# Performance work log

Hardware: AMD Instinct MI355X
Metric: run time of the kernel (lower is better)

Reference implementation:

```python
import jax, jax.numpy as jnp
import numpy as np

N_QUBITS = 12
N_LAYERS = 2
PATCH = 16
NPS = 14  # patches per side for 224/16
N_PATCHES = NPS * NPS
SCALE = 1.0 / np.sqrt(N_QUBITS)


def _butterfly_gates(n):
    # Faithful replication of QuantumOrthogonalLayer.butterfly_circuit indexing:
    # param_idx increments even when the (idx1, idx2) pair is skipped.
    gates, pidx = [], 0
    n_bl = int(np.ceil(np.log2(n)))
    for layer in range(n_bl):
        stride = 2 ** layer
        for start in range(0, n - stride, 2 * stride):
            for off in range(stride):
                i1, i2 = start + off, start + off + stride
                if i1 < n and i2 < n:
                    gates.append((pidx, i1, i2))
                pidx += 1
    nppl = sum(2 ** (n_bl - 1 - i) * 2 ** i for i in range(n_bl))  # n_params() = 32
    return gates, nppl

GATES, NPPL = _butterfly_gates(N_QUBITS)

# Pauli-Z sign table: qubit 0 is the most-significant bit of the flattened state index.
_bits = (np.arange(2 ** N_QUBITS)[:, None] >> np.arange(N_QUBITS - 1, -1, -1)[None, :]) & 1
Z_SIGNS = jnp.asarray(1.0 - 2.0 * _bits, dtype=jnp.float32)  # (4096, 12)


def _rbs_u(theta):
    # 4x4 real unitary of RY(2t,w1); CNOT(w1,w2); RY(-2t,w1); CNOT(w1,w2)
    c, s = jnp.cos(theta), jnp.sin(theta)
    c2, s2, cs = c * c, s * s, c * s
    return jnp.stack([
        jnp.stack([c2, s2, -cs, cs]),
        jnp.stack([s2, c2, cs, -cs]),
        jnp.stack([cs, -cs, c2, s2]),
        jnp.stack([-cs, cs, s2, c2]),
    ])


def _apply_2q(state, U, i, j):
    # state: (P, 2, 2, ..., 2); apply U to qubit axes i, j
    st = jnp.moveaxis(state, (1 + i, 1 + j), (-2, -1))
    shp = st.shape
    st = st.reshape(shp[:-2] + (4,)) @ U.T
    return jnp.moveaxis(st.reshape(shp), (-2, -1), (1 + i, 1 + j))


@jax.checkpoint
def quantum_expvals(features, params):
    # features: (P, n_qubits) angles; params: (N_LAYERS * NPPL,)
    P = features.shape[0]
    half = 0.5 * features
    amp = jnp.stack([jnp.cos(half), jnp.sin(half)], axis=-1)  # (P, n, 2) RY(x)|0>
    state = jnp.ones((P, 1), features.dtype)
    for q in range(N_QUBITS):  # product-state angle encoding
        state = (state[:, :, None] * amp[:, q][:, None, :]).reshape(P, -1)
    state = state.reshape((P,) + (2,) * N_QUBITS)
    for l in range(N_LAYERS):
        base = l * NPPL
        for pidx, w1, w2 in GATES:
            state = _apply_2q(state, _rbs_u(params[base + pidx]), w1, w2)
    probs = state.reshape(P, -1) ** 2
    return probs @ Z_SIGNS  # (P, n_qubits) <Z_i>


def setup_inputs() -> dict:
    key = jax.random.key(0)
    ks = jax.random.split(key, 6)
    x = jax.random.normal(ks[0], (4, 3, 224, 224), dtype=jnp.float32)
    W_proj = jax.random.normal(ks[1], (N_QUBITS, PATCH * PATCH), dtype=jnp.float32) / np.sqrt(PATCH * PATCH)
    b_proj = jnp.zeros((N_QUBITS,), jnp.float32)
    q_params = 0.1 * jax.random.normal(ks[2], (N_LAYERS * NPPL,), dtype=jnp.float32)
    k_params = 0.1 * jax.random.normal(ks[3], (N_LAYERS * NPPL,), dtype=jnp.float32)
    v_params = 0.1 * jax.random.normal(ks[4], (N_LAYERS * NPPL,), dtype=jnp.float32)
    W_cls = jax.random.normal(ks[5], (1000, N_PATCHES * N_QUBITS), dtype=jnp.float32) / np.sqrt(N_PATCHES * N_QUBITS)
    b_cls = jnp.zeros((1000,), jnp.float32)
    return {"x": x, "W_proj": W_proj, "b_proj": b_proj, "q_params": q_params,
            "k_params": k_params, "v_params": v_params, "W_cls": W_cls, "b_cls": b_cls}


def reference(x, W_proj, b_proj, q_params, k_params, v_params, W_cls, b_cls):
    B = x.shape[0]
    xg = jnp.mean(x, axis=1)  # channel average -> (B, H, W)
    patches = xg.reshape(B, NPS, PATCH, NPS, PATCH).transpose(0, 1, 3, 2, 4)
    patches = patches.reshape(B, N_PATCHES, PATCH * PATCH)
    proj = patches @ W_proj.T + b_proj  # (B, n_patches, n_qubits)
    feats = proj.reshape(-1, N_QUBITS)
    Q = quantum_expvals(feats, q_params).reshape(B, N_PATCHES, N_QUBITS)
    K = quantum_expvals(feats, k_params).reshape(B, N_PATCHES, N_QUBITS)
    V = quantum_expvals(feats, v_params).reshape(B, N_PATCHES, N_QUBITS)
    attn = jax.nn.softmax(jnp.einsum('bqd,bkd->bqk', Q, K) * SCALE, axis=-1)
    out = jnp.einsum('bqk,bkd->bqd', attn, V)  # (B, n_patches, n_qubits)
    logits = out.reshape(B, -1) @ W_cls.T + b_cls
    return logits
```

## Files before the change

kernel.cpp:

```cpp
#include <hip/hip_runtime.h>
#include <math.h>

#define NQ        12
#define NPS       14
#define NPATCH    196
#define NB        4
#define NCLS      1000
#define FEATDIM   2352
#define SCALE_F   0.28867513459481287f

typedef float v2f __attribute__((ext_vector_type(2)));

constexpr int PRa[8][5] = {
    {2,3,0,1, 4},
    {2,3,4,5, 6},
    {2,3,5,6, 7},
    {2,3,0,4, 6},
    {2,3,8,9,10},
    {2,3,9,10,11},
    {2,3,0,8,10},
    {2,3,1,5, 9},
};
constexpr int PTa[8][7] = {
    {5,6,7,8,9,10,11},
    {7,0,1,8,9,10,11},
    {0,1,4,8,9,10,11},
    {8,9,10,1,5,7,11},
    {4,0,1,5,6,7,11},
    {0,1,8,5,6,7,4},
    {1,5,9,6,7,11,4},
    {6,0,11,7,8,10,4},
};
constexpr bool BARa[8] = {false,false,false,false,true,false,false,true};

constexpr int cwgt(int X, int q) {
    for (int k = 0; k < 5; ++k) if (PRa[X][k] == q) return 1 << k;
    for (int m = 0; m < 7; ++m) if (PTa[X][m] == q) return 36 << m;
    return 0;
}
constexpr int rimmB(int X, int Y, int a) {
    int s = 0;
    for (int j = 0; j < 3; ++j)
        if ((a >> j) & 1) s += cwgt(X, PRa[Y][2 + j]);
    return s;
}

template<int TI>
__device__ __forceinline__ void relayoutB(v2f amp2[16], float* lds, int tid, int base) {
    constexpr int X = TI, Y = (TI + 1) & 7;
    float4* dst = (float4*)(lds + 36 * tid);
    #pragma unroll
    for (int k = 0; k < 8; ++k)
        dst[k] = make_float4(amp2[2*k][0], amp2[2*k][1], amp2[2*k+1][0], amp2[2*k+1][1]);
    if (BARa[TI]) __syncthreads();
    #pragma unroll
    for (int a = 0; a < 8; ++a) {
        float4 v = *(const float4*)(lds + base + rimmB(X, Y, a));
        amp2[2*a][0] = v.x; amp2[2*a][1] = v.y;
        amp2[2*a+1][0] = v.z; amp2[2*a+1][1] = v.w;
    }
    if (BARa[TI]) __syncthreads();
}

template<int MI, int MJ>
__device__ __forceinline__ void pk_gate(v2f a[16], float gc, float gs) {
    v2f H = {0.5f, 0.5f}, C = {gc, gc}, S = {gs, gs};
    #pragma unroll
    for (int m = 0; m < 16; ++m) {
        if (m & (MI | MJ)) continue;
        v2f a0 = a[m], a1 = a[m | MJ], a2 = a[m | MI], a3 = a[m | MI | MJ];
        v2f p  = a0 + a1, q  = a0 - a1;
        v2f p2 = a2 + a3, q2 = a2 - a3;
        v2f t1 = H * p  + C * q  - S * q2;
        v2f t2 = H * p2 + C * q2 + S * q;
        a[m]           = t1;
        a[m | MJ]      = p  - t1;
        a[m | MI]      = t2;
        a[m | MI | MJ] = p2 - t2;
    }
}

template<int MI, int MJ>
__device__ __forceinline__ void sc_gate(float* amp, float gc, float gs) {
    #pragma unroll
    for (int m = 0; m < 32; ++m) {
        if (m & (MI | MJ)) continue;
        float a0 = amp[m], a1 = amp[m | MJ], a2 = amp[m | MI], a3 = amp[m | MI | MJ];
        float p  = a0 + a1, q  = a0 - a1;
        float p2 = a2 + a3, q2 = a2 - a3;
        float t1 = 0.5f * p  + gc * q  - gs * q2;
        float t2 = 0.5f * p2 + gc * q2 + gs * q;
        amp[m]           = t1;
        amp[m | MJ]      = p  - t1;
        amp[m | MI]      = t2;
        amp[m | MI | MJ] = p2 - t2;
    }
}

template<int CTRL>
__device__ __forceinline__ float dppadd(float x) {
    int s = __builtin_amdgcn_update_dpp(0, __float_as_int(x), CTRL, 0xf, 0xf, true);
    return x + __int_as_float(s);
}
__device__ __forceinline__ float wave_sum(float x) {
    x = dppadd<0x111>(x);
    x = dppadd<0x112>(x);
    x = dppadd<0x114>(x);
    x = dppadd<0x118>(x);
    x = dppadd<0x142>(x);
    x = dppadd<0x143>(x);
    return x;
}

__global__ __launch_bounds__(128, 4) void qcirc_kernel(
    const float* __restrict__ x,
    const float* __restrict__ Wp,
    const float* __restrict__ bproj,
    const float* __restrict__ qp,
    const float* __restrict__ kp,
    const float* __restrict__ vp,
    float* __restrict__ qkv)
{
    __shared__ __align__(16) float lds[4608];
    __shared__ float chs[NQ], shs[NQ];
    __shared__ float gC[40], gS[40];
    __shared__ float red2[2][12];

    const int tid = threadIdx.x;
    const int p = blockIdx.x, b = blockIdx.y, c = blockIdx.z;
    const int bp = b * NPATCH + p;
    const float* params = (c == 0) ? qp : (c == 1) ? kp : vp;
    const int lane = tid & 63, wv = tid >> 6;

    float part[NQ];
    #pragma unroll
    for (int q = 0; q < NQ; ++q) part[q] = 0.0f;
    {
        int py = p / NPS, px = p % NPS;
        const float* xb = x + (size_t)b * 3 * 224 * 224;
        #pragma unroll
        for (int k = 0; k < 2; ++k) {
            int pix = tid + 128 * k;
            int off = (py * 16 + (pix >> 4)) * 224 + px * 16 + (pix & 15);
            float v = (xb[off] + xb[off + 50176] + xb[off + 100352]) * (1.0f / 3.0f);
            #pragma unroll
            for (int q = 0; q < NQ; ++q) part[q] += v * Wp[q * 256 + pix];
        }
    }
    if (tid < 40) {
        int l = tid / 20, g = tid - l * 20;
        float th = params[l * 32 + g];
        gC[tid] = 0.5f * cosf(2.0f * th);
        gS[tid] = 0.5f * sinf(2.0f * th);
    }
    #pragma unroll
    for (int q = 0; q < NQ; ++q) part[q] = wave_sum(part[q]);
    if (lane == 63) {
        #pragma unroll
        for (int q = 0; q < NQ; ++q) red2[wv][q] = part[q];
    }
    __syncthreads();
    if (tid < NQ) {
        float h = 0.5f * (red2[0][tid] + red2[1][tid] + bproj[tid]);
        chs[tid] = cosf(h); shs[tid] = sinf(h);
    }
    __syncthreads();

    int baseT[8];
    #pragma unroll
    for (int TI = 0; TI < 8; ++TI) {
        int Y = (TI + 1) & 7, s = 0;
        #pragma unroll
        for (int j = 0; j < 7; ++j)
            s += ((tid >> j) & 1) ? cwgt(TI, PTa[Y][j]) : 0;
        baseT[TI] = s;
    }

    v2f amp2[16];
    float* amp = (float*)amp2;
    {
        float hi = ((tid &  1) ? shs[5]  : chs[5])  *
                   ((tid &  2) ? shs[6]  : chs[6])  *
                   ((tid &  4) ? shs[7]  : chs[7])  *
                   ((tid &  8) ? shs[8]  : chs[8])  *
                   ((tid & 16) ? shs[9]  : chs[9])  *
                   ((tid & 32) ? shs[10] : chs[10]) *
                   ((tid & 64) ? shs[11] : chs[11]);
        float pA[8], pB[4];
        #pragma unroll
        for (int i = 0; i < 8; ++i)
            pA[i] = ((i & 1) ? shs[2] : chs[2]) * ((i & 2) ? shs[3] : chs[3]) *
                    ((i & 4) ? shs[0] : chs[0]);
        #pragma unroll
        for (int i = 0; i < 4; ++i)
            pB[i] = ((i & 1) ? shs[1] : chs[1]) * ((i & 2) ? shs[4] : chs[4]);
        #pragma unroll
        for (int r = 0; r < 32; ++r) amp[r] = pA[r & 7] * pB[r >> 3] * hi;
    }

    #pragma unroll 1
    for (int l = 0; l < 2; ++l) {
        const int bb = l * 20;
        pk_gate<2, 4>(amp2, gC[bb+0], gS[bb+0]);
        sc_gate<1, 2>(amp,  gC[bb+1], gS[bb+1]);
        sc_gate<4, 1>(amp,  gC[bb+6], gS[bb+6]);
        pk_gate<4, 1>(amp2, gC[bb+7], gS[bb+7]);
        relayoutB<0>(amp2, lds, tid, baseT[0]);
        pk_gate<2, 4>(amp2, gC[bb+2], gS[bb+2]);
        relayoutB<1>(amp2, lds, tid, baseT[1]);
        pk_gate<4, 8>(amp2, gC[bb+3],  gS[bb+3]);
        pk_gate<2, 8>(amp2, gC[bb+9],  gS[bb+9]);
        pk_gate<1, 8>(amp2, gC[bb+15], gS[bb+15]);
        relayoutB<2>(amp2, lds, tid, baseT[2]);
        pk_gate<4, 8>(amp2, gC[bb+8],  gS[bb+8]);
        pk_gate<2, 4>(amp2, gC[bb+12], gS[bb+12]);
        sc_gate<1,16>(amp,  gC[bb+14], gS[bb+14]);
        relayoutB<3>(amp2, lds, tid, baseT[3]);
        pk_gate<2, 4>(amp2, gC[bb+4], gS[bb+4]);
        relayoutB<4>(amp2, lds, tid, baseT[4]);
        pk_gate<4, 8>(amp2, gC[bb+5],  gS[bb+5]);
        pk_gate<2, 8>(amp2, gC[bb+11], gS[bb+11]);
        pk_gate<1, 8>(amp2, gC[bb+19], gS[bb+19]);
        relayoutB<5>(amp2, lds, tid, baseT[5]);
        pk_gate<4, 8>(amp2, gC[bb+10], gS[bb+10]);
        pk_gate<2, 4>(amp2, gC[bb+16], gS[bb+16]);
        sc_gate<1,16>(amp,  gC[bb+18], gS[bb+18]);
        relayoutB<6>(amp2, lds, tid, baseT[6]);
        pk_gate<2, 4>(amp2, gC[bb+13], gS[bb+13]);
        pk_gate<2, 8>(amp2, gC[bb+17], gS[bb+17]);
        if (l == 0) relayoutB<7>(amp2, lds, tid, baseT[7]);
    }

    float T, Sq2, Sq3, Sq1, Sq5, Sq9;
    {
        float t1[16]; Sq2 = 0.0f;
        #pragma unroll
        for (int i = 0; i < 16; ++i) {
            float e = amp[2*i] * amp[2*i], o = amp[2*i+1] * amp[2*i+1];
            t1[i] = e + o; Sq2 += e - o;
        }
        float t2[8]; Sq3 = 0.0f;
        #pragma unroll
        for (int i = 0; i < 8; ++i) { t2[i] = t1[2*i] + t1[2*i+1]; Sq3 += t1[2*i] - t1[2*i+1]; }
        float t3[4]; Sq1 = 0.0f;
        #pragma unroll
        for (int i = 0; i < 4; ++i) { t3[i] = t2[2*i] + t2[2*i+1]; Sq1 += t2[2*i] - t2[2*i+1]; }
        float t4[2]; Sq5 = 0.0f;
        #pragma unroll
        for (int i = 0; i < 2; ++i) { t4[i] = t3[2*i] + t3[2*i+1]; Sq5 += t3[2*i] - t3[2*i+1]; }
        T = t4[0] + t4[1]; Sq9 = t4[0] - t4[1];
    }
    float Vq6  = (tid &  1) ? -T : T;
    float Vq0  = (tid &  2) ? -T : T;
    float Vq11 = (tid &  4) ? -T : T;
    float Vq7  = (tid &  8) ? -T : T;
    float Vq8  = (tid & 16) ? -T : T;
    float Vq10 = (tid & 32) ? -T : T;
    T    = wave_sum(T);
    Vq6  = wave_sum(Vq6);  Vq0  = wave_sum(Vq0);  Vq11 = wave_sum(Vq11);
    Vq7  = wave_sum(Vq7);  Vq8  = wave_sum(Vq8);  Vq10 = wave_sum(Vq10);
    Sq2  = wave_sum(Sq2);  Sq3  = wave_sum(Sq3);  Sq1  = wave_sum(Sq1);
    Sq5  = wave_sum(Sq5);  Sq9  = wave_sum(Sq9);
    if (lane == 63) {
        red2[wv][0]  = Vq0;  red2[wv][1]  = Sq1;  red2[wv][2]  = Sq2;
        red2[wv][3]  = Sq3;  red2[wv][4]  = T;    red2[wv][5]  = Sq5;
        red2[wv][6]  = Vq6;  red2[wv][7]  = Vq7;  red2[wv][8]  = Vq8;
        red2[wv][9]  = Sq9;  red2[wv][10] = Vq10; red2[wv][11] = Vq11;
    }
    __syncthreads();
    if (tid < NQ) {
        float v1 = red2[1][tid];
        float s = red2[0][tid] + ((tid == 4) ? -v1 : v1);
        qkv[((size_t)c * (NB * NPATCH) + bp) * NQ + tid] = s;
    }
}

__global__ __launch_bounds__(256) void attn_kernel(
    const float* __restrict__ qkv,
    float* __restrict__ outb)
{
    int tid = threadIdx.x;
    int qp = blockIdx.x, b = blockIdx.y;
    const float* Q = qkv;
    const float* K = qkv + NB * NPATCH * NQ;
    const float* V = qkv + 2 * NB * NPATCH * NQ;

    __shared__ float redm[4], reds[4], redv[4][NQ];

    float4 q0 = ((const float4*)(Q + (b * NPATCH + qp) * NQ))[0];
    float4 q1 = ((const float4*)(Q + (b * NPATCH + qp) * NQ))[1];
    float4 q2 = ((const float4*)(Q + (b * NPATCH + qp) * NQ))[2];

    float score = -1e30f;
    float4 v0, v1, v2;
    if (tid < NPATCH) {
        const float4* K4 = (const float4*)(K + (b * NPATCH + tid) * NQ);
        float4 k0 = K4[0], k1 = K4[1], k2 = K4[2];
        float s = q0.x*k0.x + q0.y*k0.y + q0.z*k0.z + q0.w*k0.w
                + q1.x*k1.x + q1.y*k1.y + q1.z*k1.z + q1.w*k1.w
                + q2.x*k2.x + q2.y*k2.y + q2.z*k2.z + q2.w*k2.w;
        score = s * SCALE_F;
        const float4* V4 = (const float4*)(V + (b * NPATCH + tid) * NQ);
        v0 = V4[0]; v1 = V4[1]; v2 = V4[2];
    }
    float m = score;
    #pragma unroll
    for (int o = 32; o > 0; o >>= 1) m = fmaxf(m, __shfl_down(m, o));
    int lane = tid & 63, wv = tid >> 6;
    if (lane == 0) redm[wv] = m;
    __syncthreads();
    float maxv = fmaxf(fmaxf(redm[0], redm[1]), fmaxf(redm[2], redm[3]));

    float w = (tid < NPATCH) ? expf(score - maxv) : 0.0f;
    float sm = w;
    #pragma unroll
    for (int o = 32; o > 0; o >>= 1) sm += __shfl_down(sm, o);
    if (lane == 0) reds[wv] = sm;

    float part[NQ];
    #pragma unroll
    for (int d = 0; d < NQ; d++) part[d] = 0.0f;
    if (tid < NPATCH) {
        part[0] = w*v0.x; part[1] = w*v0.y; part[2]  = w*v0.z; part[3]  = w*v0.w;
        part[4] = w*v1.x; part[5] = w*v1.y; part[6]  = w*v1.z; part[7]  = w*v1.w;
        part[8] = w*v2.x; part[9] = w*v2.y; part[10] = w*v2.z; part[11] = w*v2.w;
    }
    #pragma unroll
    for (int d = 0; d < NQ; d++) {
        #pragma unroll
        for (int o = 32; o > 0; o >>= 1) part[d] += __shfl_down(part[d], o);
    }
    if (lane == 0) {
        #pragma unroll
        for (int d = 0; d < NQ; d++) redv[wv][d] = part[d];
    }
    __syncthreads();
    if (tid < NQ) {
        float sumv = reds[0] + reds[1] + reds[2] + reds[3];
        float s = redv[0][tid] + redv[1][tid] + redv[2][tid] + redv[3][tid];
        outb[(size_t)b * FEATDIM + qp * NQ + tid] = s / sumv;
    }
}

__global__ __launch_bounds__(256) void cls_kernel(
    const float* __restrict__ outb,
    const float* __restrict__ Wc,
    const float* __restrict__ bc,
    float* __restrict__ logits)
{
    int o = blockIdx.x, tid = threadIdx.x;
    float acc[NB] = {0.0f, 0.0f, 0.0f, 0.0f};
    const float4* w4 = (const float4*)(Wc + (size_t)o * FEATDIM);
    for (int j = tid; j < FEATDIM / 4; j += 256) {
        float4 w = w4[j];
        #pragma unroll
        for (int b = 0; b < NB; b++) {
            float4 ov = ((const float4*)(outb + (size_t)b * FEATDIM))[j];
            acc[b] += w.x*ov.x + w.y*ov.y + w.z*ov.z + w.w*ov.w;
        }
    }
    #pragma unroll
    for (int b = 0; b < NB; b++) {
        #pragma unroll
        for (int off = 32; off > 0; off >>= 1) acc[b] += __shfl_down(acc[b], off);
    }
    __shared__ float red[4][NB];
    int lane = tid & 63, wv = tid >> 6;
    if (lane == 0) {
        #pragma unroll
        for (int b = 0; b < NB; b++) red[wv][b] = acc[b];
    }
    __syncthreads();
    if (tid < NB) {
        float s = red[0][tid] + red[1][tid] + red[2][tid] + red[3][tid];
        logits[(size_t)tid * NCLS + o] = s + bc[o];
    }
}

extern "C" void kernel_launch(void* const* d_in, const int* in_sizes, int n_in,
                              void* d_out, int out_size, void* d_ws, size_t ws_size,
                              hipStream_t stream) {
    const float* x     = (const float*)d_in[0];
    const float* Wp    = (const float*)d_in[1];
    const float* bproj = (const float*)d_in[2];
    const float* qp    = (const float*)d_in[3];
    const float* kp    = (const float*)d_in[4];
    const float* vp    = (const float*)d_in[5];
    const float* Wc    = (const float*)d_in[6];
    const float* bc    = (const float*)d_in[7];
    float* logits = (float*)d_out;

    float* ws   = (float*)d_ws;
    float* qkv  = ws;
    float* outb = ws + 28224;

    qcirc_kernel<<<dim3(NPATCH, NB, 3), 128, 0, stream>>>(x, Wp, bproj, qp, kp, vp, qkv);
    attn_kernel <<<dim3(NPATCH, NB),    256, 0, stream>>>(qkv, outb);
    cls_kernel  <<<NCLS,                256, 0, stream>>>(outb, Wc, bc, logits);
}
```

Before: 116.1 us.

## Split LDS relayout into two half-passes to shrink shared memory per block

The register-to-LDS relayout now stages half of each thread's 32 amplitudes at a time, with a 20-float stride instead of 36, so the shared buffer shrinks from 4608 to 2560 floats. Each relayout becomes two write/read phases that split on one qubit, either a register slot or a thread bit, and add extra barriers in some stages. The launch bound rises from 4 to 7 waves per SIMD so the smaller LDS footprint can give more resident blocks. In exchange it adds LDS round trips, more synchronisation and an 8-entry float4 staging array that raises register pressure.

```diff
diff --git a/kernel.cpp b/kernel.cpp
--- a/kernel.cpp
+++ b/kernel.cpp
@@ -33,33 +33,94 @@
 };
 constexpr bool BARa[8] = {false,false,false,false,true,false,false,true};
 
-constexpr int cwgt(int X, int q) {
-    for (int k = 0; k < 5; ++k) if (PRa[X][k] == q) return 1 << k;
-    for (int m = 0; m < 7; ++m) if (PTa[X][m] == q) return 36 << m;
+constexpr int STRIDE = 20;
+
+constexpr int cwgt2(int X, int q) {
+    for (int k = 0; k < 4; ++k) if (PRa[X][k] == q) return 1 << k;
+    if (PRa[X][4] == q) return 0;
+    for (int m = 0; m < 7; ++m) if (PTa[X][m] == q) return STRIDE << m;
     return 0;
 }
-constexpr int rimmB(int X, int Y, int a) {
+constexpr int rimm2(int X, int Y, int a) {
     int s = 0;
     for (int j = 0; j < 3; ++j)
-        if ((a >> j) & 1) s += cwgt(X, PRa[Y][2 + j]);
+        if ((a >> j) & 1) s += cwgt2(X, PRa[Y][2 + j]);
     return s;
 }
+constexpr int splitpos(int X) {
+    int Y = (X + 1) & 7, H = PRa[X][4];
+    for (int j = 0; j < 3; ++j) if (PRa[Y][2 + j] == H) return j;
+    for (int m = 0; m < 7; ++m) if (PTa[Y][m] == H) return 8 + m;
+    return -1;
+}
 
 template<int TI>
-__device__ __forceinline__ void relayoutB(v2f amp2[16], float* lds, int tid, int base) {
+__device__ __forceinline__ void relayout2(v2f amp2[16], float* lds, int tid, int base) {
     constexpr int X = TI, Y = (TI + 1) & 7;
-    float4* dst = (float4*)(lds + 36 * tid);
-    #pragma unroll
-    for (int k = 0; k < 8; ++k)
+    constexpr int SP = splitpos(TI);
+    constexpr bool BAR = BARa[TI];
+    float4* dst = (float4*)(lds + STRIDE * tid);
+
+    #pragma unroll
+    for (int k = 0; k < 4; ++k)
         dst[k] = make_float4(amp2[2*k][0], amp2[2*k][1], amp2[2*k+1][0], amp2[2*k+1][1]);
-    if (BARa[TI]) __syncthreads();
-    #pragma unroll
-    for (int a = 0; a < 8; ++a) {
-        float4 v = *(const float4*)(lds + base + rimmB(X, Y, a));
-        amp2[2*a][0] = v.x; amp2[2*a][1] = v.y;
-        amp2[2*a+1][0] = v.z; amp2[2*a+1][1] = v.w;
-    }
-    if (BARa[TI]) __syncthreads();
+    if (BAR) __syncthreads();
+
+    if constexpr (SP < 3) {
+        float4 rv[8];
+        #pragma unroll
+        for (int a = 0; a < 8; ++a)
+            if (!((a >> SP) & 1))
+                rv[a] = *(const float4*)(lds + base + rimm2(X, Y, a));
+        if (BAR) __syncthreads();
+        #pragma unroll
+        for (int k = 0; k < 4; ++k)
+            dst[k] = make_float4(amp2[8+2*k][0], amp2[8+2*k][1], amp2[9+2*k][0], amp2[9+2*k][1]);
+        #pragma unroll
+        for (int a = 0; a < 8; ++a)
+            if (!((a >> SP) & 1)) {
+                amp2[2*a][0]   = rv[a].x; amp2[2*a][1]   = rv[a].y;
+                amp2[2*a+1][0] = rv[a].z; amp2[2*a+1][1] = rv[a].w;
+            }
+        if (BAR) __syncthreads();
+        #pragma unroll
+        for (int a = 0; a < 8; ++a)
+            if ((a >> SP) & 1) {
+                float4 v = *(const float4*)(lds + base + rimm2(X, Y, a));
+                amp2[2*a][0]   = v.x; amp2[2*a][1]   = v.y;
+                amp2[2*a+1][0] = v.z; amp2[2*a+1][1] = v.w;
+            }
+        if (BAR) __syncthreads();
+    } else {
+        constexpr int TB = SP - 8;
+        const bool p0 = ((tid >> TB) & 1) == 0;
+        float4 rv[8];
+        if (p0) {
+            #pragma unroll
+            for (int a = 0; a < 8; ++a)
+                rv[a] = *(const float4*)(lds + base + rimm2(X, Y, a));
+        }
+        if (BAR) __syncthreads();
+        #pragma unroll
+        for (int k = 0; k < 4; ++k)
+            dst[k] = make_float4(amp2[8+2*k][0], amp2[8+2*k][1], amp2[9+2*k][0], amp2[9+2*k][1]);
+        if (BAR) __syncthreads();
+        if (p0) {
+            #pragma unroll
+            for (int a = 0; a < 8; ++a) {
+                amp2[2*a][0]   = rv[a].x; amp2[2*a][1]   = rv[a].y;
+                amp2[2*a+1][0] = rv[a].z; amp2[2*a+1][1] = rv[a].w;
+            }
+        } else {
+            #pragma unroll
+            for (int a = 0; a < 8; ++a) {
+                float4 v = *(const float4*)(lds + base + rimm2(X, Y, a));
+                amp2[2*a][0]   = v.x; amp2[2*a][1]   = v.y;
+                amp2[2*a+1][0] = v.z; amp2[2*a+1][1] = v.w;
+            }
+        }
+        if (BAR) __syncthreads();
+    }
 }
 
 template<int MI, int MJ>
@@ -112,7 +173,7 @@
     return x;
 }
 
-__global__ __launch_bounds__(128, 4) void qcirc_kernel(
+__global__ __launch_bounds__(128, 7) void qcirc_kernel(
     const float* __restrict__ x,
     const float* __restrict__ Wp,
     const float* __restrict__ bproj,
@@ -121,7 +182,7 @@
     const float* __restrict__ vp,
     float* __restrict__ qkv)
 {
-    __shared__ __align__(16) float lds[4608];
+    __shared__ __align__(16) float lds[STRIDE * 128];
     __shared__ float chs[NQ], shs[NQ];
     __shared__ float gC[40], gS[40];
     __shared__ float red2[2][12];
@@ -172,7 +233,7 @@
         int Y = (TI + 1) & 7, s = 0;
         #pragma unroll
         for (int j = 0; j < 7; ++j)
-            s += ((tid >> j) & 1) ? cwgt(TI, PTa[Y][j]) : 0;
+            s += ((tid >> j) & 1) ? cwgt2(TI, PTa[Y][j]) : 0;
         baseT[TI] = s;
     }
 
@@ -205,30 +266,30 @@
         sc_gate<1, 2>(amp,  gC[bb+1], gS[bb+1]);
         sc_gate<4, 1>(amp,  gC[bb+6], gS[bb+6]);
         pk_gate<4, 1>(amp2, gC[bb+7], gS[bb+7]);
-        relayoutB<0>(amp2, lds, tid, baseT[0]);
+        relayout2<0>(amp2, lds, tid, baseT[0]);
         pk_gate<2, 4>(amp2, gC[bb+2], gS[bb+2]);
-        relayoutB<1>(amp2, lds, tid, baseT[1]);
+        relayout2<1>(amp2, lds, tid, baseT[1]);
         pk_gate<4, 8>(amp2, gC[bb+3],  gS[bb+3]);
         pk_gate<2, 8>(amp2, gC[bb+9],  gS[bb+9]);
         pk_gate<1, 8>(amp2, gC[bb+15], gS[bb+15]);
-        relayoutB<2>(amp2, lds, tid, baseT[2]);
+        relayout2<2>(amp2, lds, tid, baseT[2]);
         pk_gate<4, 8>(amp2, gC[bb+8],  gS[bb+8]);
         pk_gate<2, 4>(amp2, gC[bb+12], gS[bb+12]);
         sc_gate<1,16>(amp,  gC[bb+14], gS[bb+14]);
-        relayoutB<3>(amp2, lds, tid, baseT[3]);
+        relayout2<3>(amp2, lds, tid, baseT[3]);
         pk_gate<2, 4>(amp2, gC[bb+4], gS[bb+4]);
-        relayoutB<4>(amp2, lds, tid, baseT[4]);
+        relayout2<4>(amp2, lds, tid, baseT[4]);
         pk_gate<4, 8>(amp2, gC[bb+5],  gS[bb+5]);
         pk_gate<2, 8>(amp2, gC[bb+11], gS[bb+11]);
         pk_gate<1, 8>(amp2, gC[bb+19], gS[bb+19]);
-        relayoutB<5>(amp2, lds, tid, baseT[5]);
+        relayout2<5>(amp2, lds, tid, baseT[5]);
         pk_gate<4, 8>(amp2, gC[bb+10], gS[bb+10]);
         pk_gate<2, 4>(amp2, gC[bb+16], gS[bb+16]);
         sc_gate<1,16>(amp,  gC[bb+18], gS[bb+18]);
-        relayoutB<6>(amp2, lds, tid, baseT[6]);
+        relayout2<6>(amp2, lds, tid, baseT[6]);
         pk_gate<2, 4>(amp2, gC[bb+13], gS[bb+13]);
         pk_gate<2, 8>(amp2, gC[bb+17], gS[bb+17]);
-        if (l == 0) relayoutB<7>(amp2, lds, tid, baseT[7]);
+        if (l == 0) relayout2<7>(amp2, lds, tid, baseT[7]);
     }
 
     float T, Sq2, Sq3, Sq1, Sq5, Sq9;
```

After: 129.3 us. 1.11x slower.
